# Kernel optimization log

Measured on AMD Instinct MI355X. Metric: run time of the kernel, lower is better.

The kernel has to match this reference:

```python
import jax, jax.numpy as jnp
import numpy as np

S, I, H, C, B = 512, 1, 256, 10, 2048

def _xavier(key, shape):
    fan_out, fan_in = shape
    std = (2.0 / (fan_in + fan_out)) ** 0.5
    return jax.random.normal(key, shape, dtype=jnp.float32) * std

def setup_inputs() -> dict:
    key = jax.random.key(0)
    k_x, k_hx, k_hh, k_ph = jax.random.split(key, 4)
    return {
        "x": jax.random.normal(k_x, (B, S), dtype=jnp.float32),
        "W_hx": _xavier(k_hx, (H, I)),
        "W_hh": _xavier(k_hh, (H, H)),
        "W_ph": _xavier(k_ph, (C, H)),
        "b_h": jnp.zeros((H, 1), dtype=jnp.float32),
        "b_p": jnp.zeros((C, 1), dtype=jnp.float32),
    }

def reference(x, W_hx, W_hh, W_ph, b_h, b_p):
    # x: [B, S]; hidden state h: [H, B]
    batch = x.shape[0]
    h0 = jnp.zeros((W_hh.shape[0], batch), dtype=x.dtype)
    xs = x.T  # [S, B], one row per timestep

    def step(h, x_t):
        # x_t: [B] -> [1, B]; W_hx: [H, 1]
        h_new = jnp.tanh(W_hx @ x_t[None, :] + W_hh @ h + b_h)
        return h_new, None

    h_final, _ = jax.lax.scan(step, h0, xs)
    # output: [B, C]
    return (W_ph @ h_final + b_p).T
```

## Files before the change

kernel.cpp:

```cpp
#include <hip/hip_runtime.h>


#define SEQ    512
#define HID    256
#define NCLS   10
#define BN     16
#define NT     512
#define XP     17
#define PITCH  264

typedef _Float16 f16x8 __attribute__((ext_vector_type(8)));
typedef _Float16 f16x4 __attribute__((ext_vector_type(4)));
typedef float    f32x4 __attribute__((ext_vector_type(4)));

#define MFMA16(a, b, c) __builtin_amdgcn_mfma_f32_16x16x32_f16(a, b, c, 0, 0, 0)

__global__ __launch_bounds__(NT)
__attribute__((amdgpu_waves_per_eu(2, 2)))
void rnn_mfma(
    const float* __restrict__ x,
    const float* __restrict__ W_hx,
    const float* __restrict__ W_hh,
    const float* __restrict__ W_ph,
    const float* __restrict__ b_h,
    const float* __restrict__ b_p,
    float* __restrict__ out)
{
    __shared__ __align__(16) _Float16 hT[2][BN][PITCH];
    __shared__ __align__(16) float xs[SEQ + 2][XP];

    const int tid  = threadIdx.x;
    const int lane = tid & 63;
    const int wave = tid >> 6;
    const int n16  = lane & 15;
    const int quad = lane >> 4;
    const int b0   = blockIdx.x * BN;

    const float SC = 2.885390081777926814f;

    f16x8 afrag[2][8];
#pragma unroll
    for (int mt = 0; mt < 2; ++mt) {
        const int row = wave * 32 + mt * 16 + n16;
#pragma unroll
        for (int ks = 0; ks < 8; ++ks) {
            const float4* p = (const float4*)&W_hh[row * HID + ks * 32 + quad * 8];
            float4 u = p[0], v = p[1];
            f16x8 a;
            a[0] = (_Float16)(SC * u.x); a[1] = (_Float16)(SC * u.y);
            a[2] = (_Float16)(SC * u.z); a[3] = (_Float16)(SC * u.w);
            a[4] = (_Float16)(SC * v.x); a[5] = (_Float16)(SC * v.y);
            a[6] = (_Float16)(SC * v.z); a[7] = (_Float16)(SC * v.w);
            afrag[mt][ks] = a;
        }
    }
    f32x4 bias[2], wxv[2];
#pragma unroll
    for (int mt = 0; mt < 2; ++mt)
#pragma unroll
        for (int r = 0; r < 4; ++r) {
            const int row = wave * 32 + mt * 16 + quad * 4 + r;
            bias[mt][r] = SC * b_h[row];
            wxv[mt][r]  = SC * W_hx[row];
        }

    const int rbase = n16 * (PITCH * 2) + quad * 16;
    const int wbase = n16 * (PITCH * 2) + wave * 64 + quad * 8;

    for (int i = tid; i < BN * SEQ / 4; i += NT) {
        const int n = i >> 7, t4 = (i & 127) * 4;
        float4 v = *(const float4*)&x[(b0 + n) * SEQ + t4];
        xs[t4 + 0][n] = v.x; xs[t4 + 1][n] = v.y;
        xs[t4 + 2][n] = v.z; xs[t4 + 3][n] = v.w;
    }
    for (int i = tid; i < BN * PITCH / 2; i += NT) ((float*)hT[0])[i] = 0.0f;
    __syncthreads();

    float xv = xs[0][n16];

#define RNN_STEP(T, RD, WR, P)                                                \
    {                                                                         \
        const float xnxt = xs[(T) + 1][n16];      \
        const char* rb = (const char*)hT[RD] + rbase;                         \
        char*       wb = (char*)hT[WR] + wbase;                               \
                                                \
        f16x8 bA0 = *(const f16x8*)(rb + (((P) + 0) & 7) * 64);               \
        f16x8 bA1 = *(const f16x8*)(rb + (((P) + 1) & 7) * 64);               \
        f16x8 bA2 = *(const f16x8*)(rb + (((P) + 2) & 7) * 64);               \
        f16x8 bA3 = *(const f16x8*)(rb + (((P) + 3) & 7) * 64);               \
        f32x4 acc[2];                                                         \
        _Pragma("unroll")                                                     \
        for (int mt = 0; mt < 2; ++mt) {                                      \
            f32x4 c0;                                                         \
            _Pragma("unroll")                                                 \
            for (int r = 0; r < 4; ++r)                                       \
                c0[r] = fmaf(wxv[mt][r], xv, bias[mt][r]);                    \
            acc[mt] = MFMA16(afrag[mt][((P) + 0) & 7], bA0, c0);              \
        }                                                                     \
        acc[0] = MFMA16(afrag[0][((P) + 1) & 7], bA1, acc[0]);                \
        acc[1] = MFMA16(afrag[1][((P) + 1) & 7], bA1, acc[1]);                \
                                      \
        f16x8 bB0 = *(const f16x8*)(rb + (((P) + 4) & 7) * 64);               \
        f16x8 bB1 = *(const f16x8*)(rb + (((P) + 5) & 7) * 64);               \
        f16x8 bB2 = *(const f16x8*)(rb + (((P) + 6) & 7) * 64);               \
        f16x8 bB3 = *(const f16x8*)(rb + (((P) + 7) & 7) * 64);               \
        acc[0] = MFMA16(afrag[0][((P) + 2) & 7], bA2, acc[0]);                \
        acc[1] = MFMA16(afrag[1][((P) + 2) & 7], bA2, acc[1]);                \
        acc[0] = MFMA16(afrag[0][((P) + 3) & 7], bA3, acc[0]);                \
        acc[1] = MFMA16(afrag[1][((P) + 3) & 7], bA3, acc[1]);                \
        acc[0] = MFMA16(afrag[0][((P) + 4) & 7], bB0, acc[0]);                \
        acc[1] = MFMA16(afrag[1][((P) + 4) & 7], bB0, acc[1]);                \
        acc[0] = MFMA16(afrag[0][((P) + 5) & 7], bB1, acc[0]);                \
        acc[1] = MFMA16(afrag[1][((P) + 5) & 7], bB1, acc[1]);                \
        acc[0] = MFMA16(afrag[0][((P) + 6) & 7], bB2, acc[0]);                \
        acc[1] = MFMA16(afrag[1][((P) + 6) & 7], bB2, acc[1]);                \
        acc[0] = MFMA16(afrag[0][((P) + 7) & 7], bB3, acc[0]);                \
        acc[1] = MFMA16(afrag[1][((P) + 7) & 7], bB3, acc[1]);                \
        _Pragma("unroll")                                                     \
        for (int mt = 0; mt < 2; ++mt) {                                      \
            f16x4 h4;                                                         \
            _Pragma("unroll")                                                 \
            for (int r = 0; r < 4; ++r) {                                     \
                float ex = __builtin_amdgcn_exp2f(acc[mt][r]);                \
                float rc = __builtin_amdgcn_rcpf(ex + 1.0f);                  \
                h4[r] = (_Float16)(1.0f - 2.0f * rc);                         \
            }                                                                 \
            *(f16x4*)(wb + mt * 32) = h4;                                     \
        }                                                                     \
        xv = xnxt;                                                            \
        __syncthreads();                                                      \
    }

    if (((wave >> 2) & 1) == 0) {
        for (int t = 0; t < SEQ; t += 2) {
            RNN_STEP(t,     0, 1, 0)
            RNN_STEP(t + 1, 1, 0, 0)
        }
    } else {
        for (int t = 0; t < SEQ; t += 2) {
            RNN_STEP(t,     0, 1, 4)
            RNN_STEP(t + 1, 1, 0, 4)
        }
    }
#undef RNN_STEP

    if (tid < BN * NCLS) {
        const int b = tid / NCLS, c = tid % NCLS;
        float sum = b_p[c];
        const _Float16* hp = hT[0][b];
        for (int j = 0; j < HID; ++j)
            sum += W_ph[c * HID + j] * (float)hp[j];
        out[(b0 + b) * NCLS + c] = sum;
    }
}

extern "C" void kernel_launch(void* const* d_in, const int* in_sizes, int n_in,
                              void* d_out, int out_size, void* d_ws, size_t ws_size,
                              hipStream_t stream) {
    const float* x    = (const float*)d_in[0];
    const float* W_hx = (const float*)d_in[1];
    const float* W_hh = (const float*)d_in[2];
    const float* W_ph = (const float*)d_in[3];
    const float* b_h  = (const float*)d_in[4];
    const float* b_p  = (const float*)d_in[5];
    float* out = (float*)d_out;

    rnn_mfma<<<dim3(2048 / BN), dim3(NT), 0, stream>>>(
        x, W_hx, W_hh, W_ph, b_h, b_p, out);
}
```

Before: 332.4 us.

## Halve block to 4 waves, each computing 64 rows with split-K accumulators

The block shrinks from 8 to 4 waves, so each wave now holds four 16-row tiles of W_hh in registers and issues 32 MFMAs per step. The reduction is split into two independent accumulator chains (even and odd K halves) that are summed before the tanh, which shortens the dependent MFMA chain. The per-wave rotated LDS read order is dropped, and the x staging pitch changes. Fewer waves mean cheaper barriers each step, in exchange for more registers per wave (occupancy pinned to 1 wave per EU), less latency hiding, and a single all-waves-same-order LDS read pattern.

```diff
diff --git a/kernel.cpp b/kernel.cpp
--- a/kernel.cpp
+++ b/kernel.cpp
@@ -5,8 +5,8 @@
 #define HID    256
 #define NCLS   10
 #define BN     16
-#define NT     512
-#define XP     17
+#define NT     256
+#define XP     41
 #define PITCH  264
 
 typedef _Float16 f16x8 __attribute__((ext_vector_type(8)));
@@ -16,7 +16,7 @@
 #define MFMA16(a, b, c) __builtin_amdgcn_mfma_f32_16x16x32_f16(a, b, c, 0, 0, 0)
 
 __global__ __launch_bounds__(NT)
-__attribute__((amdgpu_waves_per_eu(2, 2)))
+__attribute__((amdgpu_waves_per_eu(1, 1)))
 void rnn_mfma(
     const float* __restrict__ x,
     const float* __restrict__ W_hx,
@@ -38,10 +38,10 @@
 
     const float SC = 2.885390081777926814f;
 
-    f16x8 afrag[2][8];
+    f16x8 afrag[4][8];
 #pragma unroll
-    for (int mt = 0; mt < 2; ++mt) {
-        const int row = wave * 32 + mt * 16 + n16;
+    for (int mt = 0; mt < 4; ++mt) {
+        const int row = wave * 64 + mt * 16 + n16;
 #pragma unroll
         for (int ks = 0; ks < 8; ++ks) {
             const float4* p = (const float4*)&W_hh[row * HID + ks * 32 + quad * 8];
@@ -54,18 +54,18 @@
             afrag[mt][ks] = a;
         }
     }
-    f32x4 bias[2], wxv[2];
+    f32x4 bias[4], wxv[4];
 #pragma unroll
-    for (int mt = 0; mt < 2; ++mt)
+    for (int mt = 0; mt < 4; ++mt)
 #pragma unroll
         for (int r = 0; r < 4; ++r) {
-            const int row = wave * 32 + mt * 16 + quad * 4 + r;
+            const int row = wave * 64 + mt * 16 + quad * 4 + r;
             bias[mt][r] = SC * b_h[row];
             wxv[mt][r]  = SC * W_hx[row];
         }
 
     const int rbase = n16 * (PITCH * 2) + quad * 16;
-    const int wbase = n16 * (PITCH * 2) + wave * 64 + quad * 8;
+    const int wbase = n16 * (PITCH * 2) + wave * 128 + quad * 8;
 
     for (int i = tid; i < BN * SEQ / 4; i += NT) {
         const int n = i >> 7, t4 = (i & 127) * 4;
@@ -78,50 +78,56 @@
 
     float xv = xs[0][n16];
 
-#define RNN_STEP(T, RD, WR, P)                                                \
+#define RNN_STEP(T, RD, WR)                                                   \
     {                                                                         \
         const float xnxt = xs[(T) + 1][n16];      \
         const char* rb = (const char*)hT[RD] + rbase;                         \
         char*       wb = (char*)hT[WR] + wbase;                               \
-                                                \
-        f16x8 bA0 = *(const f16x8*)(rb + (((P) + 0) & 7) * 64);               \
-        f16x8 bA1 = *(const f16x8*)(rb + (((P) + 1) & 7) * 64);               \
-        f16x8 bA2 = *(const f16x8*)(rb + (((P) + 2) & 7) * 64);               \
-        f16x8 bA3 = *(const f16x8*)(rb + (((P) + 3) & 7) * 64);               \
-        f32x4 acc[2];                                                         \
+        f16x8 f0 = *(const f16x8*)(rb + 0 * 64);                              \
+        f16x8 f1 = *(const f16x8*)(rb + 1 * 64);                              \
+        f16x8 f2 = *(const f16x8*)(rb + 2 * 64);                              \
+        f16x8 f3 = *(const f16x8*)(rb + 3 * 64);                              \
+        f16x8 f4 = *(const f16x8*)(rb + 4 * 64);                              \
+        f16x8 f5 = *(const f16x8*)(rb + 5 * 64);                              \
+        f16x8 f6 = *(const f16x8*)(rb + 6 * 64);                              \
+        f16x8 f7 = *(const f16x8*)(rb + 7 * 64);                              \
+        f32x4 e[4], o[4];                    \
         _Pragma("unroll")                                                     \
-        for (int mt = 0; mt < 2; ++mt) {                                      \
+        for (int mt = 0; mt < 4; ++mt) {                                      \
             f32x4 c0;                                                         \
             _Pragma("unroll")                                                 \
             for (int r = 0; r < 4; ++r)                                       \
                 c0[r] = fmaf(wxv[mt][r], xv, bias[mt][r]);                    \
-            acc[mt] = MFMA16(afrag[mt][((P) + 0) & 7], bA0, c0);              \
+            e[mt] = MFMA16(afrag[mt][0], f0, c0);                             \
         }                                                                     \
-        acc[0] = MFMA16(afrag[0][((P) + 1) & 7], bA1, acc[0]);                \
-        acc[1] = MFMA16(afrag[1][((P) + 1) & 7], bA1, acc[1]);                \
-                                      \
-        f16x8 bB0 = *(const f16x8*)(rb + (((P) + 4) & 7) * 64);               \
-        f16x8 bB1 = *(const f16x8*)(rb + (((P) + 5) & 7) * 64);               \
-        f16x8 bB2 = *(const f16x8*)(rb + (((P) + 6) & 7) * 64);               \
-        f16x8 bB3 = *(const f16x8*)(rb + (((P) + 7) & 7) * 64);               \
-        acc[0] = MFMA16(afrag[0][((P) + 2) & 7], bA2, acc[0]);                \
-        acc[1] = MFMA16(afrag[1][((P) + 2) & 7], bA2, acc[1]);                \
-        acc[0] = MFMA16(afrag[0][((P) + 3) & 7], bA3, acc[0]);                \
-        acc[1] = MFMA16(afrag[1][((P) + 3) & 7], bA3, acc[1]);                \
-        acc[0] = MFMA16(afrag[0][((P) + 4) & 7], bB0, acc[0]);                \
-        acc[1] = MFMA16(afrag[1][((P) + 4) & 7], bB0, acc[1]);                \
-        acc[0] = MFMA16(afrag[0][((P) + 5) & 7], bB1, acc[0]);                \
-        acc[1] = MFMA16(afrag[1][((P) + 5) & 7], bB1, acc[1]);                \
-        acc[0] = MFMA16(afrag[0][((P) + 6) & 7], bB2, acc[0]);                \
-        acc[1] = MFMA16(afrag[1][((P) + 6) & 7], bB2, acc[1]);                \
-        acc[0] = MFMA16(afrag[0][((P) + 7) & 7], bB3, acc[0]);                \
-        acc[1] = MFMA16(afrag[1][((P) + 7) & 7], bB3, acc[1]);                \
         _Pragma("unroll")                                                     \
-        for (int mt = 0; mt < 2; ++mt) {                                      \
+        for (int mt = 0; mt < 4; ++mt)                                        \
+            o[mt] = MFMA16(afrag[mt][4], f4, (f32x4)0.0f);                    \
+        _Pragma("unroll")                                                     \
+        for (int mt = 0; mt < 4; ++mt)                                        \
+            e[mt] = MFMA16(afrag[mt][1], f1, e[mt]);                          \
+        _Pragma("unroll")                                                     \
+        for (int mt = 0; mt < 4; ++mt)                                        \
+            o[mt] = MFMA16(afrag[mt][5], f5, o[mt]);                          \
+        _Pragma("unroll")                                                     \
+        for (int mt = 0; mt < 4; ++mt)                                        \
+            e[mt] = MFMA16(afrag[mt][2], f2, e[mt]);                          \
+        _Pragma("unroll")                                                     \
+        for (int mt = 0; mt < 4; ++mt)                                        \
+            o[mt] = MFMA16(afrag[mt][6], f6, o[mt]);                          \
+        _Pragma("unroll")                                                     \
+        for (int mt = 0; mt < 4; ++mt)                                        \
+            e[mt] = MFMA16(afrag[mt][3], f3, e[mt]);                          \
+        _Pragma("unroll")                                                     \
+        for (int mt = 0; mt < 4; ++mt)                                        \
+            o[mt] = MFMA16(afrag[mt][7], f7, o[mt]);                          \
+        _Pragma("unroll")                                                     \
+        for (int mt = 0; mt < 4; ++mt) {                                      \
             f16x4 h4;                                                         \
             _Pragma("unroll")                                                 \
             for (int r = 0; r < 4; ++r) {                                     \
-                float ex = __builtin_amdgcn_exp2f(acc[mt][r]);                \
+                float s  = e[mt][r] + o[mt][r];                               \
+                float ex = __builtin_amdgcn_exp2f(s);                         \
                 float rc = __builtin_amdgcn_rcpf(ex + 1.0f);                  \
                 h4[r] = (_Float16)(1.0f - 2.0f * rc);                         \
             }                                                                 \
@@ -131,16 +137,9 @@
         __syncthreads();                                                      \
     }
 
-    if (((wave >> 2) & 1) == 0) {
-        for (int t = 0; t < SEQ; t += 2) {
-            RNN_STEP(t,     0, 1, 0)
-            RNN_STEP(t + 1, 1, 0, 0)
-        }
-    } else {
-        for (int t = 0; t < SEQ; t += 2) {
-            RNN_STEP(t,     0, 1, 4)
-            RNN_STEP(t + 1, 1, 0, 4)
-        }
+    for (int t = 0; t < SEQ; t += 2) {
+        RNN_STEP(t, 0, 1)
+        RNN_STEP(t + 1, 1, 0)
     }
 #undef RNN_STEP
 
```

New measurement: 422.4 us. 1.27x slower.
